# Kernel optimization log

Hardware: AMD Instinct MI355X
Metric: run time of the kernel (lower is better)

Reference implementation:

```python
import jax, jax.numpy as jnp
import numpy as np

D_MODEL = 1024
N_HEADS = 16
D_K = D_MODEL // N_HEADS
NEG = -1e9


def setup_inputs() -> dict:
    key = jax.random.key(0)
    ks = jax.random.split(key, 6)
    B, T, D = 4, 2048, D_MODEL
    s = 1.0 / np.sqrt(D)
    x = jax.random.normal(ks[0], (B, T, D), dtype=jnp.float32)
    Wq = jax.random.normal(ks[1], (D, D), dtype=jnp.float32) * s
    Wk = jax.random.normal(ks[2], (D, D), dtype=jnp.float32) * s
    Wv = jax.random.normal(ks[3], (D, D), dtype=jnp.float32) * s
    Wo = jax.random.normal(ks[4], (D, D), dtype=jnp.float32) * s
    bo = jnp.zeros((D,), dtype=jnp.float32)
    # causal mask: True above diagonal = masked (masked_fill where True)
    mask = jnp.triu(jnp.ones((T, T), dtype=bool), k=1)
    return {"x": x, "mask": mask, "Wq": Wq, "Wk": Wk, "Wv": Wv, "Wo": Wo, "bo": bo}


def reference(x, mask, Wq, Wk, Wv, Wo, bo):
    B, T, D = x.shape
    # torch nn.Linear: y = x @ W.T
    q = (x @ Wq.T).reshape(B, T, N_HEADS, D_K).transpose(0, 2, 1, 3)  # [B,H,T,dk]
    k = (x @ Wk.T).reshape(B, T, N_HEADS, D_K).transpose(0, 2, 1, 3)
    v = (x @ Wv.T).reshape(B, T, N_HEADS, D_K).transpose(0, 2, 1, 3)
    scores = jnp.einsum("bhqd,bhkd->bhqk", q, k) / np.sqrt(D_K)  # [B,H,T,T]
    scores = jnp.where(mask[:T, :T], NEG, scores)
    attn = jax.nn.softmax(scores, axis=-1)
    ctx = jnp.einsum("bhqk,bhkd->bhqd", attn, v)  # [B,H,T,dk]
    ctx = ctx.transpose(0, 2, 1, 3).reshape(B, T, D)
    return ctx @ Wo.T + bo
```

## Files before the change

### kernel.cpp

```cpp
#include <hip/hip_runtime.h>
#include <hip/hip_bf16.h>


typedef __attribute__((ext_vector_type(8))) short bf16x8;
typedef __attribute__((ext_vector_type(4))) float f32x4;

__device__ __forceinline__ unsigned short f2b(float x) {
  __hip_bfloat16 h = __float2bfloat16(x);
  return __builtin_bit_cast(unsigned short, h);
}

__device__ __forceinline__ void load_lds16(const void* g, void* l) {
  __builtin_amdgcn_global_load_lds((__attribute__((address_space(1))) void*)g,
                                   (__attribute__((address_space(3))) void*)l,
                                   16, 0, 0);
}

__global__ void cast_kernel(const float* __restrict__ x,
                            const float* __restrict__ w0, const float* __restrict__ w1,
                            const float* __restrict__ w2, const float* __restrict__ w3,
                            unsigned short* __restrict__ xb, unsigned short* __restrict__ wb) {
  int i = blockIdx.x * 256 + threadIdx.x;
  const float* src;
  unsigned short* dst;
  int c;
  if (i < 1048576) {
    src = x; dst = xb; c = i;
  } else {
    int cw = i - 1048576;
    int wi = cw >> 17;
    c = cw & 131071;
    src = (wi == 0) ? w0 : (wi == 1) ? w1 : (wi == 2) ? w2 : w3;
    dst = wb + ((size_t)wi << 20);
  }
  const float4* s4 = (const float4*)src;
  float4 a = s4[2 * c], b = s4[2 * c + 1];
  union { unsigned short u[8]; uint4 v; } r;
  r.u[0] = f2b(a.x); r.u[1] = f2b(a.y); r.u[2] = f2b(a.z); r.u[3] = f2b(a.w);
  r.u[4] = f2b(b.x); r.u[5] = f2b(b.y); r.u[6] = f2b(b.z); r.u[7] = f2b(b.w);
  ((uint4*)dst)[c] = r.v;
}

__launch_bounds__(512, 2)
__global__ void gemm_qkv(const unsigned short* __restrict__ A,
                         const unsigned short* __restrict__ Bw,
                         unsigned short* __restrict__ Cout) {
  __shared__ unsigned short At[3][256 * 64];
  __shared__ unsigned short Bt[3][128 * 64];

  const int tid = threadIdx.x;
  const int lane = tid & 63;
  const int w = tid >> 6;
  const int quad = lane >> 4;
  const int l15 = lane & 15;
  const int m0 = blockIdx.x * 256;
  const int n0 = blockIdx.y * 128;
  const int wm = (w & 3) * 64;
  const int wn = (w >> 2) * 64;

  auto stageA = [&](int buf, int kt, int c) {
    int chunk = c * 512 + tid;
    int row = chunk >> 3;
    int scol = (chunk & 7) ^ (row & 7);
    load_lds16(A + (size_t)(m0 + row) * 1024 + kt + scol * 8,
               &At[buf][(c * 512 + (w << 6)) << 3]);
  };
  auto stageB = [&](int buf, int kt, int c) {
    int chunk = c * 512 + tid;
    int row = chunk >> 3;
    int scol = (chunk & 7) ^ (row & 7);
    load_lds16(Bw + (size_t)(n0 + row) * 1024 + kt + scol * 8,
               &Bt[buf][(c * 512 + (w << 6)) << 3]);
  };

  const f32x4 z4 = {0.f, 0.f, 0.f, 0.f};
  f32x4 acc[4][4];
#pragma unroll
  for (int i = 0; i < 4; ++i)
#pragma unroll
    for (int j = 0; j < 4; ++j) acc[i][j] = z4;

#pragma unroll
  for (int c = 0; c < 4; ++c) stageA(0, 0, c);
#pragma unroll
  for (int c = 0; c < 2; ++c) stageB(0, 0, c);
#pragma unroll
  for (int c = 0; c < 4; ++c) stageA(1, 64, c);
#pragma unroll
  for (int c = 0; c < 2; ++c) stageB(1, 64, c);
  asm volatile("s_waitcnt vmcnt(6)" ::: "memory");
  __builtin_amdgcn_s_barrier();
  __builtin_amdgcn_sched_barrier(0);

  int buf = 0;
  for (int t = 0; t < 16; ++t) {
    const int sbuf = (buf >= 1) ? buf - 1 : 2;
    const int skt = (t + 2) * 64;
    const bool st = (t < 14);

    {
      bf16x8 a0[4], b0[4];
#pragma unroll
      for (int i = 0; i < 4; ++i) {
        int rowA = wm + i * 16 + l15;
        a0[i] = *(const bf16x8*)&At[buf][rowA * 64 + ((quad ^ (rowA & 7)) << 3)];
      }
#pragma unroll
      for (int j = 0; j < 4; ++j) {
        int rowB = wn + j * 16 + l15;
        b0[j] = *(const bf16x8*)&Bt[buf][rowB * 64 + ((quad ^ (rowB & 7)) << 3)];
      }
      if (st) { stageA(sbuf, skt, 0); stageA(sbuf, skt, 1); stageA(sbuf, skt, 2); }
      __builtin_amdgcn_s_barrier();
      asm volatile("s_waitcnt lgkmcnt(0)" ::: "memory");
      __builtin_amdgcn_sched_barrier(0);
      __builtin_amdgcn_s_setprio(1);
#pragma unroll
      for (int i = 0; i < 4; ++i)
#pragma unroll
        for (int j = 0; j < 4; ++j)
          acc[i][j] = __builtin_amdgcn_mfma_f32_16x16x32_bf16(a0[i], b0[j], acc[i][j], 0, 0, 0);
      __builtin_amdgcn_s_setprio(0);
      __builtin_amdgcn_s_barrier();
      __builtin_amdgcn_sched_barrier(0);
    }

    {
      bf16x8 a1[4], b1[4];
#pragma unroll
      for (int i = 0; i < 4; ++i) {
        int rowA = wm + i * 16 + l15;
        a1[i] = *(const bf16x8*)&At[buf][rowA * 64 + (((4 + quad) ^ (rowA & 7)) << 3)];
      }
#pragma unroll
      for (int j = 0; j < 4; ++j) {
        int rowB = wn + j * 16 + l15;
        b1[j] = *(const bf16x8*)&Bt[buf][rowB * 64 + (((4 + quad) ^ (rowB & 7)) << 3)];
      }
      if (st) { stageA(sbuf, skt, 3); stageB(sbuf, skt, 0); stageB(sbuf, skt, 1); }
      __builtin_amdgcn_s_barrier();
      asm volatile("s_waitcnt lgkmcnt(0)" ::: "memory");
      __builtin_amdgcn_sched_barrier(0);
      __builtin_amdgcn_s_setprio(1);
#pragma unroll
      for (int i = 0; i < 4; ++i)
#pragma unroll
        for (int j = 0; j < 4; ++j)
          acc[i][j] = __builtin_amdgcn_mfma_f32_16x16x32_bf16(a1[i], b1[j], acc[i][j], 0, 0, 0);
      __builtin_amdgcn_s_setprio(0);
      if (t < 14) {
        asm volatile("s_waitcnt vmcnt(6)" ::: "memory");
      } else if (t == 14) {
        asm volatile("s_waitcnt vmcnt(0)" ::: "memory");
      }
      __builtin_amdgcn_s_barrier();
      __builtin_amdgcn_sched_barrier(0);
    }

    buf = (buf < 2) ? buf + 1 : 0;
  }

  const int seg = n0 >> 10;
#pragma unroll
  for (int i = 0; i < 4; ++i) {
#pragma unroll
    for (int j = 0; j < 4; ++j) {
#pragma unroll
      for (int r = 0; r < 4; ++r) {
        int m = m0 + wm + i * 16 + quad * 4 + r;
        int n = n0 + wn + j * 16 + l15;
        int nn = n & 1023;
        float v = acc[i][j][r];
        if (seg == 0) {
          Cout[(size_t)m * 1024 + nn] = f2b(v);
        } else if (seg == 1) {
          (Cout + 8388608)[(size_t)m * 1024 + nn] = f2b(v);
        } else {
          int b = m >> 11, tq = m & 2047, hh = nn >> 6, d = nn & 63;
          (Cout + 16777216)[(((size_t)((b * 16 + hh) * 64 + d)) << 11) + tq] = f2b(v);
        }
      }
    }
  }
}

__launch_bounds__(256)
__global__ void gemm_proj(const unsigned short* __restrict__ A,
                          const unsigned short* __restrict__ Bw,
                          const float* __restrict__ bias,
                          float* __restrict__ out) {
  __shared__ unsigned short At[128 * 64];
  __shared__ unsigned short Bt[64 * 64];

  const int tid = threadIdx.x;
  const int lane = tid & 63;
  const int w = tid >> 6;
  const int quad = lane >> 4;
  const int l15 = lane & 15;
  const int m0 = blockIdx.x * 128;
  const int n0 = blockIdx.y * 64;
  const int wm = w * 32;

  const f32x4 z4 = {0.f, 0.f, 0.f, 0.f};
  f32x4 acc[2][4];
#pragma unroll
  for (int i = 0; i < 2; ++i)
#pragma unroll
    for (int j = 0; j < 4; ++j) acc[i][j] = z4;

  for (int kt = 0; kt < 1024; kt += 64) {
    __syncthreads();
#pragma unroll
    for (int c = 0; c < 4; ++c) {
      int chunk = c * 256 + tid;
      int row = chunk >> 3;
      int scol = (chunk & 7) ^ (row & 7);
      load_lds16(A + (size_t)(m0 + row) * 1024 + kt + scol * 8,
                 &At[((c * 256 + (w << 6)) << 3)]);
    }
#pragma unroll
    for (int c = 0; c < 2; ++c) {
      int chunk = c * 256 + tid;
      int row = chunk >> 3;
      int scol = (chunk & 7) ^ (row & 7);
      load_lds16(Bw + (size_t)(n0 + row) * 1024 + kt + scol * 8,
                 &Bt[((c * 256 + (w << 6)) << 3)]);
    }
    __syncthreads();
#pragma unroll
    for (int ks = 0; ks < 2; ++ks) {
      bf16x8 af[2], bf[4];
#pragma unroll
      for (int i = 0; i < 2; ++i) {
        int rowA = wm + i * 16 + l15;
        af[i] = *(const bf16x8*)&At[rowA * 64 + (((ks * 4 + quad) ^ (rowA & 7)) << 3)];
      }
#pragma unroll
      for (int j = 0; j < 4; ++j) {
        int rowB = j * 16 + l15;
        bf[j] = *(const bf16x8*)&Bt[rowB * 64 + (((ks * 4 + quad) ^ (rowB & 7)) << 3)];
      }
#pragma unroll
      for (int i = 0; i < 2; ++i)
#pragma unroll
        for (int j = 0; j < 4; ++j)
          acc[i][j] = __builtin_amdgcn_mfma_f32_16x16x32_bf16(af[i], bf[j], acc[i][j], 0, 0, 0);
    }
  }

#pragma unroll
  for (int i = 0; i < 2; ++i)
#pragma unroll
    for (int j = 0; j < 4; ++j) {
      int n = n0 + j * 16 + l15;
      float bv = bias[n];
#pragma unroll
      for (int r = 0; r < 4; ++r) {
        int m = m0 + wm + i * 16 + quad * 4 + r;
        out[(size_t)m * 1024 + n] = acc[i][j][r] + bv;
      }
    }
}

__launch_bounds__(256)
__global__ void attn_kernel(const unsigned short* __restrict__ Q,
                            const unsigned short* __restrict__ K,
                            const unsigned short* __restrict__ VT,
                            unsigned short* __restrict__ ctx) {
  __shared__ unsigned short Kt[2][64 * 64];
  __shared__ unsigned short Vt[2][64 * 64];
  __shared__ unsigned short Pt[128 * 64];

  const int tid = threadIdx.x;
  const int lane = tid & 63;
  const int w = tid >> 6;
  const int quad = lane >> 4;
  const int l15 = lane & 15;
  const int bh = blockIdx.x;
  const int pp = blockIdx.y;
  const int b = bh >> 4, h = bh & 15;

  const unsigned short* Kg = K + ((size_t)(b * 2048)) * 1024 + h * 64;
  const unsigned short* Vg = VT + ((size_t)bh * 64) * 2048;

  const float SC = 0.1803368801f;
  const float M0 = 11.0f;

  for (int tt = 0; tt < 2; ++tt) {
    const int qt = tt ? (15 - pp) : pp;
    const int qb = qt * 128;
    const int jn = 2 * qt + 2;

    bf16x8 qa[2][2];
#pragma unroll
    for (int g = 0; g < 2; ++g) {
      const unsigned short* qbase =
          Q + ((size_t)(b * 2048 + qb + w * 32 + g * 16 + l15)) * 1024 + h * 64;
      qa[g][0] = *(const bf16x8*)(qbase + quad * 8);
      qa[g][1] = *(const bf16x8*)(qbase + 32 + quad * 8);
    }

    const f32x4 z4 = {0.f, 0.f, 0.f, 0.f};
    f32x4 o[2][4];
#pragma unroll
    for (int g = 0; g < 2; ++g)
#pragma unroll
      for (int nt = 0; nt < 4; ++nt) o[g][nt] = z4;
    float lrow[2] = {0.f, 0.f};

    if (tt) __syncthreads();

#pragma unroll
    for (int c = 0; c < 2; ++c) {
      int chunk = c * 256 + tid;
      int row = chunk >> 3;
      int scol = (chunk & 7) ^ (row & 7);
      load_lds16(Kg + (size_t)row * 1024 + scol * 8, &Kt[0][((c * 256 + (w << 6)) << 3)]);
      load_lds16(Vg + ((size_t)row << 11) + scol * 8, &Vt[0][((c * 256 + (w << 6)) << 3)]);
    }

    int cur = 0;
    for (int j = 0; j < jn; ++j) {
      const int j0 = j * 64;
      __syncthreads();

      if (j + 1 < jn) {
        const int nj0 = j0 + 64;
#pragma unroll
        for (int c = 0; c < 2; ++c) {
          int chunk = c * 256 + tid;
          int row = chunk >> 3;
          int scol = (chunk & 7) ^ (row & 7);
          load_lds16(Kg + (size_t)(nj0 + row) * 1024 + scol * 8,
                     &Kt[cur ^ 1][((c * 256 + (w << 6)) << 3)]);
          load_lds16(Vg + ((size_t)row << 11) + nj0 + scol * 8,
                     &Vt[cur ^ 1][((c * 256 + (w << 6)) << 3)]);
        }
      }

      f32x4 st[2][4];
#pragma unroll
      for (int g = 0; g < 2; ++g)
#pragma unroll
        for (int nt = 0; nt < 4; ++nt) st[g][nt] = z4;
#pragma unroll
      for (int ks = 0; ks < 2; ++ks) {
#pragma unroll
        for (int nt = 0; nt < 4; ++nt) {
          int rowK = nt * 16 + l15;
          bf16x8 kf = *(const bf16x8*)&Kt[cur][rowK * 64 + (((ks * 4 + quad) ^ (rowK & 7)) << 3)];
          st[0][nt] = __builtin_amdgcn_mfma_f32_16x16x32_bf16(kf, qa[0][ks], st[0][nt], 0, 0, 0);
          st[1][nt] = __builtin_amdgcn_mfma_f32_16x16x32_bf16(kf, qa[1][ks], st[1][nt], 0, 0, 0);
        }
      }

#pragma unroll
      for (int g = 0; g < 2; ++g) {
        const int qmin = qb + w * 32 + g * 16;
        const bool dg = (j0 + 63 > qmin);
        const int q = qmin + l15;
        float sum = 0.f;
#pragma unroll
        for (int nt = 0; nt < 4; ++nt) {
#pragma unroll
          for (int r = 0; r < 4; ++r) {
            float e = fmaf(st[g][nt][r], SC, -M0);
            if (dg) {
              int kpos = j0 + nt * 16 + quad * 4 + r;
              if (kpos > q) e = -1e30f;
            }
            float pv = __builtin_amdgcn_exp2f(e);
            st[g][nt][r] = pv;
            sum += pv;
          }
        }
        sum += __shfl_xor(sum, 16);
        sum += __shfl_xor(sum, 32);
        lrow[g] += sum;
      }

#pragma unroll
      for (int g = 0; g < 2; ++g) {
        const int qrow = w * 32 + g * 16 + l15;
#pragma unroll
        for (int nt = 0; nt < 4; ++nt) {
          ushort4 pk;
          pk.x = f2b(st[g][nt][0]); pk.y = f2b(st[g][nt][1]);
          pk.z = f2b(st[g][nt][2]); pk.w = f2b(st[g][nt][3]);
          int chunk = nt * 4 + quad;
          *(ushort4*)&Pt[qrow * 64 + ((chunk ^ l15) << 2)] = pk;
        }
      }

#pragma unroll
      for (int ks = 0; ks < 2; ++ks) {
        int c0 = ks * 8 + quad * 2;
        union { ushort4 hh[2]; bf16x8 v; } pu[2];
#pragma unroll
        for (int g = 0; g < 2; ++g) {
          const int qrow = w * 32 + g * 16 + l15;
          pu[g].hh[0] = *(const ushort4*)&Pt[qrow * 64 + ((c0 ^ l15) << 2)];
          pu[g].hh[1] = *(const ushort4*)&Pt[qrow * 64 + (((c0 + 1) ^ l15) << 2)];
        }
#pragma unroll
        for (int nt = 0; nt < 4; ++nt) {
          int rowV = nt * 16 + l15;
          bf16x8 vb = *(const bf16x8*)&Vt[cur][rowV * 64 + (((ks * 4 + quad) ^ (rowV & 7)) << 3)];
          o[0][nt] = __builtin_amdgcn_mfma_f32_16x16x32_bf16(pu[0].v, vb, o[0][nt], 0, 0, 0);
          o[1][nt] = __builtin_amdgcn_mfma_f32_16x16x32_bf16(pu[1].v, vb, o[1][nt], 0, 0, 0);
        }
      }
      cur ^= 1;
    }

#pragma unroll
    for (int g = 0; g < 2; ++g) {
      float lf[4];
#pragma unroll
      for (int r = 0; r < 4; ++r) lf[r] = 1.f / __shfl(lrow[g], quad * 4 + r);
#pragma unroll
      for (int nt = 0; nt < 4; ++nt) {
#pragma unroll
        for (int r = 0; r < 4; ++r) {
          int q = qb + w * 32 + g * 16 + quad * 4 + r;
          int dcol = nt * 16 + l15;
          ctx[((size_t)(b * 2048 + q)) * 1024 + h * 64 + dcol] = f2b(o[g][nt][r] * lf[r]);
        }
      }
    }
  }
}

extern "C" void kernel_launch(void* const* d_in, const int* in_sizes, int n_in,
                              void* d_out, int out_size, void* d_ws, size_t ws_size,
                              hipStream_t stream) {
  const float* x  = (const float*)d_in[0];
  const float* Wq = (const float*)d_in[2];
  const float* Wk = (const float*)d_in[3];
  const float* Wv = (const float*)d_in[4];
  const float* Wo = (const float*)d_in[5];
  const float* bo = (const float*)d_in[6];
  float* out = (float*)d_out;

  unsigned short* xb  = (unsigned short*)d_ws;
  unsigned short* wb  = xb + 8388608;
  unsigned short* Qb  = wb + 4 * 1048576;
  unsigned short* Kb  = Qb + 8388608;
  unsigned short* VTb = Kb + 8388608;
  unsigned short* ctxb = xb;

  cast_kernel<<<6144, 256, 0, stream>>>(x, Wq, Wk, Wv, Wo, xb, wb);

  gemm_qkv<<<dim3(32, 24), 512, 0, stream>>>(xb, wb, Qb);

  attn_kernel<<<dim3(64, 8), 256, 0, stream>>>(Qb, Kb, VTb, ctxb);

  gemm_proj<<<dim3(64, 16), 256, 0, stream>>>(ctxb, wb + 3 * 1048576, bo, out);
}
```

Baseline: 275.1 us.

## Enlarge QKV GEMM tile to 256x256 with 4-stage K32 pipeline and remapped grid

The fused QKV projection GEMM moves from 256x128 tiles with a 3-buffer K=64 pipeline to 256x256 tiles with a 4-buffer K=32 pipeline. Each wave now computes a 128x64 sub-tile, which doubles the accumulators per wave. Block indices are remapped into groups of eight so neighbouring workgroups share operand tiles in cache. The intended gain is more arithmetic per LDS and global load and fewer barriers per FLOP, at the cost of higher register pressure and only 384 workgroups in the grid.

Measured after the change: 311.3 us. +13.2%, slower.

```diff
diff --git a/kernel.cpp b/kernel.cpp
--- a/kernel.cpp
+++ b/kernel.cpp
@@ -45,129 +45,116 @@
 __global__ void gemm_qkv(const unsigned short* __restrict__ A,
                          const unsigned short* __restrict__ Bw,
                          unsigned short* __restrict__ Cout) {
-  __shared__ unsigned short At[3][256 * 64];
-  __shared__ unsigned short Bt[3][128 * 64];
+  __shared__ unsigned short As[4][256 * 32];
+  __shared__ unsigned short Bs[4][256 * 32];
 
   const int tid = threadIdx.x;
   const int lane = tid & 63;
   const int w = tid >> 6;
   const int quad = lane >> 4;
   const int l15 = lane & 15;
-  const int m0 = blockIdx.x * 256;
-  const int n0 = blockIdx.y * 128;
-  const int wm = (w & 3) * 64;
-  const int wn = (w >> 2) * 64;
-
-  auto stageA = [&](int buf, int kt, int c) {
-    int chunk = c * 512 + tid;
-    int row = chunk >> 3;
-    int scol = (chunk & 7) ^ (row & 7);
-    load_lds16(A + (size_t)(m0 + row) * 1024 + kt + scol * 8,
-               &At[buf][(c * 512 + (w << 6)) << 3]);
+
+  const int flat = blockIdx.x + (blockIdx.y << 5);
+  const int wg = ((flat & 7) * 48) + (flat >> 3);
+  const int mx = wg & 31, ny = wg >> 5;
+  const int m0 = mx * 256;
+  const int n0 = ny * 256;
+  const int wm = (w >> 2) * 128;
+  const int wn = (w & 3) * 64;
+
+  auto stageA = [&](int s, int pass) {
+    int buf = s & 3;
+    int chunk = pass * 512 + tid;
+    int row = chunk >> 2;
+    int c = chunk & 3;
+    int sc = c ^ ((row >> 1) & 3);
+    load_lds16(A + (size_t)(m0 + row) * 1024 + s * 32 + sc * 8,
+               &As[buf][(pass * 512 + (w << 6)) << 3]);
   };
-  auto stageB = [&](int buf, int kt, int c) {
-    int chunk = c * 512 + tid;
-    int row = chunk >> 3;
-    int scol = (chunk & 7) ^ (row & 7);
-    load_lds16(Bw + (size_t)(n0 + row) * 1024 + kt + scol * 8,
-               &Bt[buf][(c * 512 + (w << 6)) << 3]);
+  auto stageB = [&](int s, int pass) {
+    int buf = s & 3;
+    int chunk = pass * 512 + tid;
+    int row = chunk >> 2;
+    int c = chunk & 3;
+    int sc = c ^ ((row >> 1) & 3);
+    load_lds16(Bw + (size_t)(n0 + row) * 1024 + s * 32 + sc * 8,
+               &Bs[buf][(pass * 512 + (w << 6)) << 3]);
   };
 
   const f32x4 z4 = {0.f, 0.f, 0.f, 0.f};
-  f32x4 acc[4][4];
-#pragma unroll
-  for (int i = 0; i < 4; ++i)
+  f32x4 acc[8][4];
+#pragma unroll
+  for (int i = 0; i < 8; ++i)
 #pragma unroll
     for (int j = 0; j < 4; ++j) acc[i][j] = z4;
 
 #pragma unroll
-  for (int c = 0; c < 4; ++c) stageA(0, 0, c);
-#pragma unroll
-  for (int c = 0; c < 2; ++c) stageB(0, 0, c);
-#pragma unroll
-  for (int c = 0; c < 4; ++c) stageA(1, 64, c);
-#pragma unroll
-  for (int c = 0; c < 2; ++c) stageB(1, 64, c);
-  asm volatile("s_waitcnt vmcnt(6)" ::: "memory");
+  for (int s = 0; s < 3; ++s) {
+    stageA(s, 0); stageA(s, 1); stageB(s, 0); stageB(s, 1);
+  }
+  asm volatile("s_waitcnt vmcnt(8)" ::: "memory");
   __builtin_amdgcn_s_barrier();
   __builtin_amdgcn_sched_barrier(0);
 
-  int buf = 0;
-  for (int t = 0; t < 16; ++t) {
-    const int sbuf = (buf >= 1) ? buf - 1 : 2;
-    const int skt = (t + 2) * 64;
-    const bool st = (t < 14);
-
-    {
-      bf16x8 a0[4], b0[4];
-#pragma unroll
-      for (int i = 0; i < 4; ++i) {
-        int rowA = wm + i * 16 + l15;
-        a0[i] = *(const bf16x8*)&At[buf][rowA * 64 + ((quad ^ (rowA & 7)) << 3)];
-      }
-#pragma unroll
-      for (int j = 0; j < 4; ++j) {
-        int rowB = wn + j * 16 + l15;
-        b0[j] = *(const bf16x8*)&Bt[buf][rowB * 64 + ((quad ^ (rowB & 7)) << 3)];
-      }
-      if (st) { stageA(sbuf, skt, 0); stageA(sbuf, skt, 1); stageA(sbuf, skt, 2); }
-      __builtin_amdgcn_s_barrier();
-      asm volatile("s_waitcnt lgkmcnt(0)" ::: "memory");
-      __builtin_amdgcn_sched_barrier(0);
-      __builtin_amdgcn_s_setprio(1);
-#pragma unroll
-      for (int i = 0; i < 4; ++i)
-#pragma unroll
-        for (int j = 0; j < 4; ++j)
-          acc[i][j] = __builtin_amdgcn_mfma_f32_16x16x32_bf16(a0[i], b0[j], acc[i][j], 0, 0, 0);
-      __builtin_amdgcn_s_setprio(0);
-      __builtin_amdgcn_s_barrier();
-      __builtin_amdgcn_sched_barrier(0);
-    }
-
-    {
-      bf16x8 a1[4], b1[4];
-#pragma unroll
-      for (int i = 0; i < 4; ++i) {
-        int rowA = wm + i * 16 + l15;
-        a1[i] = *(const bf16x8*)&At[buf][rowA * 64 + (((4 + quad) ^ (rowA & 7)) << 3)];
-      }
-#pragma unroll
-      for (int j = 0; j < 4; ++j) {
-        int rowB = wn + j * 16 + l15;
-        b1[j] = *(const bf16x8*)&Bt[buf][rowB * 64 + (((4 + quad) ^ (rowB & 7)) << 3)];
-      }
-      if (st) { stageA(sbuf, skt, 3); stageB(sbuf, skt, 0); stageB(sbuf, skt, 1); }
-      __builtin_amdgcn_s_barrier();
-      asm volatile("s_waitcnt lgkmcnt(0)" ::: "memory");
-      __builtin_amdgcn_sched_barrier(0);
-      __builtin_amdgcn_s_setprio(1);
-#pragma unroll
-      for (int i = 0; i < 4; ++i)
-#pragma unroll
-        for (int j = 0; j < 4; ++j)
-          acc[i][j] = __builtin_amdgcn_mfma_f32_16x16x32_bf16(a1[i], b1[j], acc[i][j], 0, 0, 0);
-      __builtin_amdgcn_s_setprio(0);
-      if (t < 14) {
-        asm volatile("s_waitcnt vmcnt(6)" ::: "memory");
-      } else if (t == 14) {
-        asm volatile("s_waitcnt vmcnt(0)" ::: "memory");
-      }
-      __builtin_amdgcn_s_barrier();
-      __builtin_amdgcn_sched_barrier(0);
-    }
-
-    buf = (buf < 2) ? buf + 1 : 0;
+  for (int t = 0; t < 32; ++t) {
+    const int buf = t & 3;
+    const bool st = (t < 29);
+    const int s3 = t + 3;
+
+    bf16x8 a0[4], a1[4], bfr[4];
+
+#pragma unroll
+    for (int i = 0; i < 4; ++i) {
+      int rowA = wm + i * 16 + l15;
+      a0[i] = *(const bf16x8*)&As[buf][rowA * 32 + ((quad ^ ((rowA >> 1) & 3)) << 3)];
+    }
+#pragma unroll
+    for (int j = 0; j < 4; ++j) {
+      int rowB = wn + j * 16 + l15;
+      bfr[j] = *(const bf16x8*)&Bs[buf][rowB * 32 + ((quad ^ ((rowB >> 1) & 3)) << 3)];
+    }
+    if (st) { stageA(s3, 0); stageA(s3, 1); }
+    __builtin_amdgcn_s_setprio(1);
+#pragma unroll
+    for (int i = 0; i < 4; ++i)
+#pragma unroll
+      for (int j = 0; j < 4; ++j)
+        acc[i][j] = __builtin_amdgcn_mfma_f32_16x16x32_bf16(a0[i], bfr[j], acc[i][j], 0, 0, 0);
+    __builtin_amdgcn_s_setprio(0);
+
+#pragma unroll
+    for (int i = 0; i < 4; ++i) {
+      int rowA = wm + 64 + i * 16 + l15;
+      a1[i] = *(const bf16x8*)&As[buf][rowA * 32 + ((quad ^ ((rowA >> 1) & 3)) << 3)];
+    }
+    if (st) { stageB(s3, 0); stageB(s3, 1); }
+    __builtin_amdgcn_s_setprio(1);
+#pragma unroll
+    for (int i = 0; i < 4; ++i)
+#pragma unroll
+      for (int j = 0; j < 4; ++j)
+        acc[4 + i][j] = __builtin_amdgcn_mfma_f32_16x16x32_bf16(a1[i], bfr[j], acc[4 + i][j], 0, 0, 0);
+    __builtin_amdgcn_s_setprio(0);
+
+    if (t < 29) {
+      asm volatile("s_waitcnt vmcnt(8)" ::: "memory");
+    } else if (t == 29) {
+      asm volatile("s_waitcnt vmcnt(4)" ::: "memory");
+    } else if (t == 30) {
+      asm volatile("s_waitcnt vmcnt(0)" ::: "memory");
+    }
+    __builtin_amdgcn_s_barrier();
+    __builtin_amdgcn_sched_barrier(0);
   }
 
   const int seg = n0 >> 10;
 #pragma unroll
-  for (int i = 0; i < 4; ++i) {
+  for (int i = 0; i < 8; ++i) {
 #pragma unroll
     for (int j = 0; j < 4; ++j) {
 #pragma unroll
       for (int r = 0; r < 4; ++r) {
-        int m = m0 + wm + i * 16 + quad * 4 + r;
+        int m = m0 + wm + (i >> 2) * 64 + (i & 3) * 16 + quad * 4 + r;
         int n = n0 + wn + j * 16 + l15;
         int nn = n & 1023;
         float v = acc[i][j][r];
@@ -451,7 +438,7 @@
 
   cast_kernel<<<6144, 256, 0, stream>>>(x, Wq, Wk, Wv, Wo, xb, wb);
 
-  gemm_qkv<<<dim3(32, 24), 512, 0, stream>>>(xb, wb, Qb);
+  gemm_qkv<<<dim3(32, 12), 512, 0, stream>>>(xb, wb, Qb);
 
   attn_kernel<<<dim3(64, 8), 256, 0, stream>>>(Qb, Kb, VTb, ctxb);
 
```

## Rewrite output projection GEMM with larger tiles and triple-buffered async pipeline

Applied to the files above, without the earlier changes.

The output projection GEMM moves from 128x64 tiles with 256 threads and a sync-load-compute loop to 256x128 tiles with 512 threads, 4x4 MFMA fragments per wave, and three LDS buffers filled ahead by direct global-to-LDS loads. This mirrors the QKV GEMM structure and aims to hide global latency and raise data reuse per tile. The intra-iteration barriers and lgkmcnt waits in the QKV GEMM (and the new proj GEMM) are also dropped, leaving one barrier per k-step. The new LDS footprint (~144KB) allows only one block per CU, and the 256-block grid fills the CUs in a single wave.

New measurement: 280.5 us. Within noise of the previous version (+2.0%).

```diff
diff --git a/kernel.cpp b/kernel.cpp
--- a/kernel.cpp
+++ b/kernel.cpp
@@ -111,9 +111,6 @@
         b0[j] = *(const bf16x8*)&Bt[buf][rowB * 64 + ((quad ^ (rowB & 7)) << 3)];
       }
       if (st) { stageA(sbuf, skt, 0); stageA(sbuf, skt, 1); stageA(sbuf, skt, 2); }
-      __builtin_amdgcn_s_barrier();
-      asm volatile("s_waitcnt lgkmcnt(0)" ::: "memory");
-      __builtin_amdgcn_sched_barrier(0);
       __builtin_amdgcn_s_setprio(1);
 #pragma unroll
       for (int i = 0; i < 4; ++i)
@@ -121,8 +118,6 @@
         for (int j = 0; j < 4; ++j)
           acc[i][j] = __builtin_amdgcn_mfma_f32_16x16x32_bf16(a0[i], b0[j], acc[i][j], 0, 0, 0);
       __builtin_amdgcn_s_setprio(0);
-      __builtin_amdgcn_s_barrier();
-      __builtin_amdgcn_sched_barrier(0);
     }
 
     {
@@ -138,9 +133,6 @@
         b1[j] = *(const bf16x8*)&Bt[buf][rowB * 64 + (((4 + quad) ^ (rowB & 7)) << 3)];
       }
       if (st) { stageA(sbuf, skt, 3); stageB(sbuf, skt, 0); stageB(sbuf, skt, 1); }
-      __builtin_amdgcn_s_barrier();
-      asm volatile("s_waitcnt lgkmcnt(0)" ::: "memory");
-      __builtin_amdgcn_sched_barrier(0);
       __builtin_amdgcn_s_setprio(1);
 #pragma unroll
       for (int i = 0; i < 4; ++i)
@@ -184,75 +176,123 @@
   }
 }
 
-__launch_bounds__(256)
+__launch_bounds__(512, 2)
 __global__ void gemm_proj(const unsigned short* __restrict__ A,
                           const unsigned short* __restrict__ Bw,
                           const float* __restrict__ bias,
                           float* __restrict__ out) {
-  __shared__ unsigned short At[128 * 64];
-  __shared__ unsigned short Bt[64 * 64];
+  __shared__ unsigned short At[3][256 * 64];
+  __shared__ unsigned short Bt[3][128 * 64];
 
   const int tid = threadIdx.x;
   const int lane = tid & 63;
   const int w = tid >> 6;
   const int quad = lane >> 4;
   const int l15 = lane & 15;
-  const int m0 = blockIdx.x * 128;
-  const int n0 = blockIdx.y * 64;
-  const int wm = w * 32;
+  const int m0 = blockIdx.x * 256;
+  const int n0 = blockIdx.y * 128;
+  const int wm = (w & 3) * 64;
+  const int wn = (w >> 2) * 64;
+
+  auto stageA = [&](int buf, int kt, int c) {
+    int chunk = c * 512 + tid;
+    int row = chunk >> 3;
+    int scol = (chunk & 7) ^ (row & 7);
+    load_lds16(A + (size_t)(m0 + row) * 1024 + kt + scol * 8,
+               &At[buf][(c * 512 + (w << 6)) << 3]);
+  };
+  auto stageB = [&](int buf, int kt, int c) {
+    int chunk = c * 512 + tid;
+    int row = chunk >> 3;
+    int scol = (chunk & 7) ^ (row & 7);
+    load_lds16(Bw + (size_t)(n0 + row) * 1024 + kt + scol * 8,
+               &Bt[buf][(c * 512 + (w << 6)) << 3]);
+  };
 
   const f32x4 z4 = {0.f, 0.f, 0.f, 0.f};
-  f32x4 acc[2][4];
-#pragma unroll
-  for (int i = 0; i < 2; ++i)
+  f32x4 acc[4][4];
+#pragma unroll
+  for (int i = 0; i < 4; ++i)
 #pragma unroll
     for (int j = 0; j < 4; ++j) acc[i][j] = z4;
 
-  for (int kt = 0; kt < 1024; kt += 64) {
-    __syncthreads();
-#pragma unroll
-    for (int c = 0; c < 4; ++c) {
-      int chunk = c * 256 + tid;
-      int row = chunk >> 3;
-      int scol = (chunk & 7) ^ (row & 7);
-      load_lds16(A + (size_t)(m0 + row) * 1024 + kt + scol * 8,
-                 &At[((c * 256 + (w << 6)) << 3)]);
-    }
-#pragma unroll
-    for (int c = 0; c < 2; ++c) {
-      int chunk = c * 256 + tid;
-      int row = chunk >> 3;
-      int scol = (chunk & 7) ^ (row & 7);
-      load_lds16(Bw + (size_t)(n0 + row) * 1024 + kt + scol * 8,
-                 &Bt[((c * 256 + (w << 6)) << 3)]);
-    }
-    __syncthreads();
-#pragma unroll
-    for (int ks = 0; ks < 2; ++ks) {
-      bf16x8 af[2], bf[4];
-#pragma unroll
-      for (int i = 0; i < 2; ++i) {
+#pragma unroll
+  for (int c = 0; c < 4; ++c) stageA(0, 0, c);
+#pragma unroll
+  for (int c = 0; c < 2; ++c) stageB(0, 0, c);
+#pragma unroll
+  for (int c = 0; c < 4; ++c) stageA(1, 64, c);
+#pragma unroll
+  for (int c = 0; c < 2; ++c) stageB(1, 64, c);
+  asm volatile("s_waitcnt vmcnt(6)" ::: "memory");
+  __builtin_amdgcn_s_barrier();
+  __builtin_amdgcn_sched_barrier(0);
+
+  int buf = 0;
+  for (int t = 0; t < 16; ++t) {
+    const int sbuf = (buf >= 1) ? buf - 1 : 2;
+    const int skt = (t + 2) * 64;
+    const bool st = (t < 14);
+
+    {
+      bf16x8 a0[4], b0[4];
+#pragma unroll
+      for (int i = 0; i < 4; ++i) {
         int rowA = wm + i * 16 + l15;
-        af[i] = *(const bf16x8*)&At[rowA * 64 + (((ks * 4 + quad) ^ (rowA & 7)) << 3)];
+        a0[i] = *(const bf16x8*)&At[buf][rowA * 64 + ((quad ^ (rowA & 7)) << 3)];
       }
 #pragma unroll
       for (int j = 0; j < 4; ++j) {
-        int rowB = j * 16 + l15;
-        bf[j] = *(const bf16x8*)&Bt[rowB * 64 + (((ks * 4 + quad) ^ (rowB & 7)) << 3)];
-      }
-#pragma unroll
-      for (int i = 0; i < 2; ++i)
+        int rowB = wn + j * 16 + l15;
+        b0[j] = *(const bf16x8*)&Bt[buf][rowB * 64 + ((quad ^ (rowB & 7)) << 3)];
+      }
+      if (st) { stageA(sbuf, skt, 0); stageA(sbuf, skt, 1); stageA(sbuf, skt, 2); }
+      __builtin_amdgcn_s_setprio(1);
+#pragma unroll
+      for (int i = 0; i < 4; ++i)
 #pragma unroll
         for (int j = 0; j < 4; ++j)
-          acc[i][j] = __builtin_amdgcn_mfma_f32_16x16x32_bf16(af[i], bf[j], acc[i][j], 0, 0, 0);
-    }
+          acc[i][j] = __builtin_amdgcn_mfma_f32_16x16x32_bf16(a0[i], b0[j], acc[i][j], 0, 0, 0);
+      __builtin_amdgcn_s_setprio(0);
+    }
+
+    {
+      bf16x8 a1[4], b1[4];
+#pragma unroll
+      for (int i = 0; i < 4; ++i) {
+        int rowA = wm + i * 16 + l15;
+        a1[i] = *(const bf16x8*)&At[buf][rowA * 64 + (((4 + quad) ^ (rowA & 7)) << 3)];
+      }
+#pragma unroll
+      for (int j = 0; j < 4; ++j) {
+        int rowB = wn + j * 16 + l15;
+        b1[j] = *(const bf16x8*)&Bt[buf][rowB * 64 + (((4 + quad) ^ (rowB & 7)) << 3)];
+      }
+      if (st) { stageA(sbuf, skt, 3); stageB(sbuf, skt, 0); stageB(sbuf, skt, 1); }
+      __builtin_amdgcn_s_setprio(1);
+#pragma unroll
+      for (int i = 0; i < 4; ++i)
+#pragma unroll
+        for (int j = 0; j < 4; ++j)
+          acc[i][j] = __builtin_amdgcn_mfma_f32_16x16x32_bf16(a1[i], b1[j], acc[i][j], 0, 0, 0);
+      __builtin_amdgcn_s_setprio(0);
+      if (t < 14) {
+        asm volatile("s_waitcnt vmcnt(6)" ::: "memory");
+      } else if (t == 14) {
+        asm volatile("s_waitcnt vmcnt(0)" ::: "memory");
+      }
+      __builtin_amdgcn_s_barrier();
+      __builtin_amdgcn_sched_barrier(0);
+    }
+
+    buf = (buf < 2) ? buf + 1 : 0;
   }
 
 #pragma unroll
-  for (int i = 0; i < 2; ++i)
+  for (int i = 0; i < 4; ++i)
 #pragma unroll
     for (int j = 0; j < 4; ++j) {
-      int n = n0 + j * 16 + l15;
+      int n = n0 + wn + j * 16 + l15;
       float bv = bias[n];
 #pragma unroll
       for (int r = 0; r < 4; ++r) {
@@ -455,5 +495,5 @@
 
   attn_kernel<<<dim3(64, 8), 256, 0, stream>>>(Qb, Kb, VTb, ctxb);
 
-  gemm_proj<<<dim3(64, 16), 256, 0, stream>>>(ctxb, wb + 3 * 1048576, bo, out);
-}
+  gemm_proj<<<dim3(32, 8), 512, 0, stream>>>(ctxb, wb + 3 * 1048576, bo, out);
+}
```
